# Kernel tuning notes

Hardware: AMD Instinct MI355X
Metric: run time of the kernel (lower is better)

The kernel has to match this reference:

```python
import jax, jax.numpy as jnp
import numpy as np

N = 240000
B = 2
GRID = (480, 360, 32)
NUM_CLASS = 20
IGNORE_LABEL = 0
MINB = np.array([0.0, -np.pi, -4.0], np.float32)
MAXB = np.array([50.0, np.pi, 2.0], np.float32)
EPS = 1e-5


def setup_inputs() -> dict:
    key = jax.random.key(0)
    ks = jax.random.split(key, 32)
    d = {}
    d['pt_fea'] = jax.random.normal(ks[0], (N, 6), jnp.float32)
    # cylindrical coords (rho, phi, z) uniformly inside the volume
    u = jax.random.uniform(ks[1], (N, 3), jnp.float32)
    d['xyz'] = u * jnp.asarray(MAXB - MINB) + jnp.asarray(MINB)
    d['batch_idx'] = jnp.sort(jax.random.randint(ks[2], (N,), 0, B)).astype(jnp.int64)
    d['pt_lab'] = jax.random.randint(ks[3], (N,), 0, NUM_CLASS).astype(jnp.int64)
    d['shuffled_ind'] = jnp.arange(N, dtype=jnp.int64)  # identity perm (deterministic)
    i = 4
    for name, c in [('bn0', 9), ('bn1', 64), ('bn2', 128), ('bn3', 256)]:
        d[name + '_g'] = jax.random.uniform(ks[i], (c,), jnp.float32, 0.5, 1.5); i += 1
        d[name + '_b'] = jax.random.normal(ks[i], (c,), jnp.float32) * 0.1; i += 1
        d[name + '_m'] = jax.random.normal(ks[i], (c,), jnp.float32) * 0.1; i += 1
        d[name + '_v'] = jax.random.uniform(ks[i], (c,), jnp.float32, 0.5, 1.5); i += 1
    for name, (fi, fo) in [('1', (9, 64)), ('2', (64, 128)), ('3', (128, 256)), ('4', (256, 256))]:
        d['w' + name] = jax.random.normal(ks[i], (fi, fo), jnp.float32) / np.sqrt(fi); i += 1
        d['b' + name] = jax.random.normal(ks[i], (fo,), jnp.float32) * 0.01; i += 1
    d['wc'] = jax.random.normal(ks[i], (256, 16), jnp.float32) / 16.0; i += 1
    d['bc'] = jax.random.normal(ks[i], (16,), jnp.float32) * 0.01
    return d


def _bn(x, g, b, m, v):
    return (x - m) * (g * jax.lax.rsqrt(v + EPS)) + b


def _ppmodel(feat, bn0_g, bn0_b, bn0_m, bn0_v, w1, b1, bn1_g, bn1_b, bn1_m, bn1_v,
             w2, b2, bn2_g, bn2_b, bn2_m, bn2_v, w3, b3, bn3_g, bn3_b, bn3_m, bn3_v, w4, b4):
    x = _bn(feat, bn0_g, bn0_b, bn0_m, bn0_v)
    x = jax.nn.relu(_bn(x @ w1 + b1, bn1_g, bn1_b, bn1_m, bn1_v))
    x = jax.nn.relu(_bn(x @ w2 + b2, bn2_g, bn2_b, bn2_m, bn2_v))
    x = jax.nn.relu(_bn(x @ w3 + b3, bn3_g, bn3_b, bn3_m, bn3_v))
    return x @ w4 + b4  # [N, 256]


def reference(pt_fea, xyz, batch_idx, pt_lab, shuffled_ind,
              bn0_g, bn0_b, bn0_m, bn0_v, w1, b1, bn1_g, bn1_b, bn1_m, bn1_v,
              w2, b2, bn2_g, bn2_b, bn2_m, bn2_v, w3, b3, bn3_g, bn3_b, bn3_m, bn3_v,
              w4, b4, wc, bc):
    minb = jnp.asarray(MINB)
    maxb = jnp.asarray(MAXB)
    grid = jnp.asarray(np.array(GRID, np.float32))
    intervals = (maxb - minb) / (grid - 1.0)

    clamped = jnp.clip(xyz, minb, maxb)
    ind = jnp.floor((clamped - minb) / intervals).astype(jnp.int32)  # [N,3]
    voxel_centers = (ind.astype(jnp.float32) + 0.5) * intervals + minb
    rel_xyz = xyz - voxel_centers
    feat = jnp.concatenate([rel_xyz, pt_fea], axis=1)  # [N,9]

    bi = batch_idx.astype(jnp.int32)
    counts = jnp.full((B,) + GRID + (NUM_CLASS,), IGNORE_LABEL, jnp.int32)
    counts = counts.at[bi, ind[:, 0], ind[:, 1], ind[:, 2], pt_lab].add(1)
    voxel_labels = jnp.argmax(counts, axis=-1).astype(jnp.int32)  # [B,480,360,32]

    feat = feat[shuffled_ind]

    flat = ((bi.astype(jnp.int64) * GRID[0] + ind[:, 0]) * GRID[1] + ind[:, 1]) * GRID[2] + ind[:, 2]
    unq, unq_inv = jnp.unique(flat, size=N, fill_value=-1, return_inverse=True)
    unq_inv = unq_inv.reshape(-1)

    processed = _ppmodel(feat, bn0_g, bn0_b, bn0_m, bn0_v, w1, b1, bn1_g, bn1_b, bn1_m, bn1_v,
                         w2, b2, bn2_g, bn2_b, bn2_m, bn2_v, w3, b3, bn3_g, bn3_b, bn3_m, bn3_v, w4, b4)
    pooled = jax.ops.segment_max(processed, unq_inv, num_segments=N)
    seg_cnt = jax.ops.segment_sum(jnp.ones((N,), jnp.float32), unq_inv, num_segments=N)
    pooled = jnp.where(seg_cnt[:, None] > 0, pooled, 0.0)  # zero out empty (padded) segments

    processed_pooled = jax.nn.relu(pooled @ wc + bc)  # fea_compression

    cat_pt_ind = jnp.concatenate([batch_idx[:, None], ind.astype(jnp.int64)], axis=1)
    return (unq, processed_pooled, voxel_labels, cat_pt_ind)
```

## Files before the change

kernel.cpp:

```cpp
#include <hip/hip_runtime.h>
#include <stdint.h>

#define N_PTS 240000
#define NV    11059200
#define NWORDS 172800
#define NB_PT 938
#define NB_WORD 675
#define NBLK_MLP 3750
#define PA 264

typedef __bf16 bf16x8 __attribute__((ext_vector_type(8)));
typedef short  short8 __attribute__((ext_vector_type(8)));
typedef float  f32x4  __attribute__((ext_vector_type(4)));

__device__ __forceinline__ unsigned short f2bf(float f) {
  unsigned u = __builtin_bit_cast(unsigned, f);
  return (unsigned short)((u + 0x7FFFu + ((u >> 16) & 1u)) >> 16);
}
__device__ __forceinline__ float bf2f(unsigned short h) {
  unsigned u = ((unsigned)h) << 16;
  return __builtin_bit_cast(float, u);
}

__device__ __forceinline__ unsigned block_sum(unsigned v, unsigned* s4, int t) {
  #pragma unroll
  for (int o = 32; o; o >>= 1) v += __shfl_down(v, o);
  if ((t & 63) == 0) s4[t >> 6] = v;
  __syncthreads();
  unsigned r = s4[0] + s4[1] + s4[2] + s4[3];
  __syncthreads();
  return r;
}

__global__ void prep_vox_kernel(
    const float* __restrict__ bng0, const float* __restrict__ bnb0, const float* __restrict__ bnm0, const float* __restrict__ bnv0,
    const float* __restrict__ bng1, const float* __restrict__ bnb1, const float* __restrict__ bnm1, const float* __restrict__ bnv1,
    const float* __restrict__ bng2, const float* __restrict__ bnb2, const float* __restrict__ bnm2, const float* __restrict__ bnv2,
    const float* __restrict__ bng3, const float* __restrict__ bnb3, const float* __restrict__ bnm3, const float* __restrict__ bnv3,
    const float* __restrict__ w1, const float* __restrict__ b1,
    const float* __restrict__ w2, const float* __restrict__ b2,
    const float* __restrict__ w3, const float* __restrict__ b3,
    const float* __restrict__ w4, const float* __restrict__ wc,
    float* __restrict__ s0, float* __restrict__ t0, float* __restrict__ w1e, float* __restrict__ be1,
    float* __restrict__ be2, float* __restrict__ be3,
    unsigned short* __restrict__ w2t, unsigned short* __restrict__ w3t, unsigned short* __restrict__ w4t,
    unsigned short* __restrict__ wct,
    const float* __restrict__ xyz, const int* __restrict__ bidx,
    unsigned* __restrict__ flatkeys, unsigned long long* __restrict__ bitmap,
    float* __restrict__ out_cat, float* __restrict__ out_unq)
{
  if (blockIdx.x < 256) {
    const int id = blockIdx.x * 256 + threadIdx.x;
    { int c = id >> 8, k = id & 255; w4t[c * 256 + k] = f2bf(w4[k * 256 + c]); }
    if (id < 32768) { int c = id >> 7, k = id & 127;
      float s = bng3[c] * rsqrtf(bnv3[c] + 1e-5f);
      w3t[c * 128 + k] = f2bf(w3[k * 256 + c] * s); }
    if (id < 8192) { int c = id >> 6, k = id & 63;
      float s = bng2[c] * rsqrtf(bnv2[c] + 1e-5f);
      w2t[c * 64 + k] = f2bf(w2[k * 128 + c] * s); }
    if (id < 4096) { int c = id >> 8, k = id & 255;
      wct[c * 256 + k] = f2bf(wc[k * 16 + c]); }
    if (id < 576) { int k = id / 64, c = id % 64;
      float s = bng1[c] * rsqrtf(bnv1[c] + 1e-5f);
      w1e[k * 64 + c] = w1[k * 64 + c] * s; }
    if (id < 64)  { float s = bng1[id] * rsqrtf(bnv1[id] + 1e-5f); be1[id] = (b1[id] - bnm1[id]) * s + bnb1[id]; }
    if (id < 128) { float s = bng2[id] * rsqrtf(bnv2[id] + 1e-5f); be2[id] = (b2[id] - bnm2[id]) * s + bnb2[id]; }
    if (id < 256) { float s = bng3[id] * rsqrtf(bnv3[id] + 1e-5f); be3[id] = (b3[id] - bnm3[id]) * s + bnb3[id]; }
    if (id < 9)   { float s = bng0[id] * rsqrtf(bnv0[id] + 1e-5f); s0[id] = s; t0[id] = bnb0[id] - bnm0[id] * s; }
    return;
  }
  const int j = (blockIdx.x - 256) * 256 + threadIdx.x;
  if (j >= N_PTS) return;
  out_unq[j] = -1.0f;
  const float PI_F = 3.14159265358979323846f;
  const float minb[3] = {0.0f, -PI_F, -4.0f};
  const float maxb[3] = {50.0f, PI_F, 2.0f};
  const float gm1[3]  = {479.0f, 359.0f, 31.0f};
  int ind[3];
  #pragma unroll
  for (int d = 0; d < 3; ++d) {
    float itv = (maxb[d] - minb[d]) / gm1[d];
    float x  = xyz[(size_t)j * 3 + d];
    float cl = fminf(fmaxf(x, minb[d]), maxb[d]);
    ind[d] = (int)floorf((cl - minb[d]) / itv);
  }
  const int bi = bidx[j];
  const unsigned flat = ((unsigned)(bi * 480 + ind[0]) * 360u + (unsigned)ind[1]) * 32u + (unsigned)ind[2];
  flatkeys[j] = flat;
  atomicOr(&bitmap[flat >> 6], 1ull << (flat & 63u));
  float* oc = out_cat + (size_t)j * 4;
  oc[0] = (float)bi; oc[1] = (float)ind[0]; oc[2] = (float)ind[1]; oc[3] = (float)ind[2];
}

__global__ void reduce_words(const unsigned long long* __restrict__ bm, unsigned* __restrict__ bsums) {
  __shared__ unsigned sh[256];
  const int w = blockIdx.x * 256 + threadIdx.x;
  sh[threadIdx.x] = (unsigned)__popcll(bm[w]);
  __syncthreads();
  for (int s = 128; s > 0; s >>= 1) { if (threadIdx.x < s) sh[threadIdx.x] += sh[threadIdx.x + s]; __syncthreads(); }
  if (threadIdx.x == 0) bsums[blockIdx.x] = sh[0];
}

__global__ __launch_bounds__(256) void scatter_unq(
    const unsigned long long* __restrict__ bm, const unsigned* __restrict__ bsums,
    unsigned* __restrict__ wordpref, unsigned* __restrict__ unqvals, float* __restrict__ out_unq)
{
  __shared__ unsigned sh[256];
  __shared__ unsigned s4[4];
  const int t = threadIdx.x, b = blockIdx.x;
  const int w = b * 256 + t;
  unsigned long long word = bm[w];
  unsigned own = (unsigned)__popcll(word);
  sh[t] = own; __syncthreads();
  for (int off = 1; off < 256; off <<= 1) {
    unsigned v = (t >= off) ? sh[t - off] : 0u;
    __syncthreads(); sh[t] += v; __syncthreads();
  }
  unsigned v = 0;
  for (int i = t; i < b; i += 256) v += bsums[i];
  const unsigned excl = block_sum(v, s4, t);
  unsigned r = excl + sh[t] - own;
  wordpref[w] = r;
  while (word) {
    int bit = __builtin_ctzll(word);
    unsigned id = (unsigned)w * 64u + (unsigned)bit;
    unqvals[r] = id;
    out_unq[r] = (float)id;
    ++r;
    word &= word - 1;
  }
}

__global__ void inv_kernel(const unsigned* __restrict__ flatkeys, const unsigned long long* __restrict__ bm,
                           const unsigned* __restrict__ wordpref,
                           unsigned* __restrict__ unq_inv, unsigned* __restrict__ cnt) {
  const int j = blockIdx.x * 256 + threadIdx.x;
  if (j >= N_PTS) return;
  const unsigned f = flatkeys[j];
  const unsigned w = f >> 6, b = f & 63u;
  const unsigned r = wordpref[w] + (unsigned)__popcll(bm[w] & ((1ull << b) - 1ull));
  unq_inv[j] = r;
  atomicAdd(&cnt[r], 1u);
}

__global__ void reduce_cnt(const unsigned* __restrict__ cnt, unsigned* __restrict__ bsums) {
  __shared__ unsigned sh[256];
  const int j = blockIdx.x * 256 + threadIdx.x;
  sh[threadIdx.x] = (j < N_PTS) ? cnt[j] : 0u;
  __syncthreads();
  for (int s = 128; s > 0; s >>= 1) { if (threadIdx.x < s) sh[threadIdx.x] += sh[threadIdx.x + s]; __syncthreads(); }
  if (threadIdx.x == 0) bsums[blockIdx.x] = sh[0];
}

__global__ __launch_bounds__(256) void scan_cnt(
    const unsigned* __restrict__ cnt, const unsigned* __restrict__ bsums,
    unsigned* __restrict__ off, unsigned* __restrict__ cur)
{
  __shared__ unsigned sh[256];
  __shared__ unsigned s4[4];
  const int t = threadIdx.x, b = blockIdx.x;
  const int j = b * 256 + t;
  unsigned own = (j < N_PTS) ? cnt[j] : 0u;
  sh[t] = own; __syncthreads();
  for (int o = 1; o < 256; o <<= 1) {
    unsigned v = (t >= o) ? sh[t - o] : 0u;
    __syncthreads(); sh[t] += v; __syncthreads();
  }
  unsigned v = 0;
  for (int i = t; i < b; i += 256) v += bsums[i];
  const unsigned excl = block_sum(v, s4, t);
  if (j < N_PTS) { unsigned e = excl + sh[t] - own; off[j] = e; cur[j] = e; }
}

__global__ void plist_fill_kernel(const unsigned* __restrict__ unq_inv, unsigned* __restrict__ cur,
                                  unsigned long long* __restrict__ plist64,
                                  const unsigned* __restrict__ cnt, const float* __restrict__ bc,
                                  float* __restrict__ out_pooled) {
  const int j = blockIdx.x * 256 + threadIdx.x;
  if (j >= N_PTS) return;
  const unsigned r = unq_inv[j];
  plist64[atomicAdd(&cur[r], 1u)] = ((unsigned long long)r << 32) | (unsigned)j;
  if (cnt[j] == 0) {
    #pragma unroll
    for (int c = 0; c < 16; ++c) out_pooled[(size_t)j * 16 + c] = fmaxf(bc[c], 0.f);
  }
}

template<int K, int C, bool RELU, bool MIDB>
__device__ __forceinline__ void gemm_stage(
    const unsigned short* __restrict__ Wt,
    const float* __restrict__ bias,
    const unsigned short* in,
    unsigned short* outp,
    int wave, int l15, int quad)
{
  constexpr int KC = K / 32;
  constexpr int NT = C / 64;
  f32x4 acc[4][NT];
  #pragma unroll
  for (int mt = 0; mt < 4; ++mt)
    #pragma unroll
    for (int nt = 0; nt < NT; ++nt) acc[mt][nt] = (f32x4){0.f, 0.f, 0.f, 0.f};
  const unsigned short* wp[NT];
  #pragma unroll
  for (int nt = 0; nt < NT; ++nt)
    wp[nt] = Wt + (size_t)(wave * 16 * NT + nt * 16 + l15) * K + quad * 8;
  bf16x8 b0[NT], b1r[NT], b2r[NT];
  #pragma unroll
  for (int nt = 0; nt < NT; ++nt)
    b0[nt] = __builtin_bit_cast(bf16x8, *(const short8*)(wp[nt]));
  if (KC > 1) {
    #pragma unroll
    for (int nt = 0; nt < NT; ++nt)
      b1r[nt] = __builtin_bit_cast(bf16x8, *(const short8*)(wp[nt] + 32));
  }
  #pragma unroll
  for (int kc = 0; kc < KC; ++kc) {
    if (kc + 2 < KC) {
      #pragma unroll
      for (int nt = 0; nt < NT; ++nt)
        b2r[nt] = __builtin_bit_cast(bf16x8, *(const short8*)(wp[nt] + (kc + 2) * 32));
    }
    __builtin_amdgcn_s_setprio(1);
    #pragma unroll
    for (int mt = 0; mt < 4; ++mt) {
      bf16x8 a = __builtin_bit_cast(bf16x8, *(const short8*)&in[(mt * 16 + l15) * PA + kc * 32 + quad * 8]);
      #pragma unroll
      for (int nt = 0; nt < NT; ++nt)
        acc[mt][nt] = __builtin_amdgcn_mfma_f32_16x16x32_bf16(b0[nt], a, acc[mt][nt], 0, 0, 0);
    }
    __builtin_amdgcn_s_setprio(0);
    #pragma unroll
    for (int nt = 0; nt < NT; ++nt) { b0[nt] = b1r[nt]; b1r[nt] = b2r[nt]; }
  }
  if (MIDB) __syncthreads();
  #pragma unroll
  for (int mt = 0; mt < 4; ++mt)
    #pragma unroll
    for (int nt = 0; nt < NT; ++nt) {
      const int cbase = wave * 16 * NT + nt * 16 + quad * 4;
      const f32x4 bs = *(const f32x4*)&bias[cbase];
      unsigned short h[4];
      #pragma unroll
      for (int r = 0; r < 4; ++r) {
        float y = acc[mt][nt][r] + bs[r];
        if (RELU) y = fmaxf(y, 0.f);
        h[r] = f2bf(y);
      }
      uint2 pk; pk.x = (unsigned)h[0] | ((unsigned)h[1] << 16);
      pk.y = (unsigned)h[2] | ((unsigned)h[3] << 16);
      *(uint2*)&outp[(mt * 16 + l15) * PA + cbase] = pk;
    }
  __syncthreads();
}

__global__ __launch_bounds__(256, 3) void mlp_pool_kernel(
    const float* __restrict__ ptfea, const float* __restrict__ xyz, const int* __restrict__ shuf,
    const unsigned long long* __restrict__ plist64,
    const unsigned* __restrict__ offv, const unsigned* __restrict__ cnt,
    const int* __restrict__ ptlab, const unsigned* __restrict__ unqvals,
    const float* __restrict__ s0, const float* __restrict__ t0,
    const float* __restrict__ w1e, const float* __restrict__ be1,
    const unsigned short* __restrict__ w2t, const float* __restrict__ be2,
    const unsigned short* __restrict__ w3t, const float* __restrict__ be3,
    const unsigned short* __restrict__ w4t, const float* __restrict__ b4,
    const unsigned short* __restrict__ wct, const float* __restrict__ bc,
    unsigned short* __restrict__ partials, float* __restrict__ out_pooled,
    float* __restrict__ out_lab)
{
  __shared__ __align__(16) unsigned short buf[64 * PA];
  __shared__ int segs[64];
  __shared__ int jrows[64];
  __shared__ int s_alast;
  __shared__ int s_nrun;
  __shared__ unsigned short s_runs[32];
  __shared__ unsigned char s_lead[64], s_comp[64];
  const int tid  = threadIdx.x;
  const int wave = tid >> 6, lane = tid & 63;
  const int l15 = lane & 15, quad = lane >> 4;
  const int row0 = blockIdx.x * 64;

  if (tid == 0) { s_alast = 0; s_nrun = 0; }
  if (lane < 16) {
    const int r = wave * 16 + lane;
    const unsigned long long v = plist64[row0 + r];
    jrows[r] = (int)(unsigned)v;
    segs[r]  = (int)(unsigned)(v >> 32);
  }

  {
    const int r = wave * 16 + (lane >> 2), part = lane & 3;
    const int sj = shuf[jrows[r]];
    const float PI_F = 3.14159265358979323846f;
    const float minb[3] = {0.0f, -PI_F, -4.0f};
    const float maxb[3] = {50.0f, PI_F, 2.0f};
    const float gm1[3]  = {479.0f, 359.0f, 31.0f};
    float x0[9];
    #pragma unroll
    for (int d = 0; d < 3; ++d) {
      float itv = (maxb[d] - minb[d]) / gm1[d];
      float x   = xyz[(size_t)sj * 3 + d];
      float cl  = fminf(fmaxf(x, minb[d]), maxb[d]);
      float fi  = floorf((cl - minb[d]) / itv);
      float center = (fi + 0.5f) * itv + minb[d];
      x0[d] = (x - center) * s0[d] + t0[d];
    }
    #pragma unroll
    for (int d = 0; d < 6; ++d) x0[3 + d] = ptfea[(size_t)sj * 6 + d] * s0[3 + d] + t0[3 + d];
    unsigned short h[16];
    #pragma unroll
    for (int ci = 0; ci < 16; ++ci) {
      float acc = be1[part * 16 + ci];
      #pragma unroll
      for (int k = 0; k < 9; ++k) acc += x0[k] * w1e[k * 64 + part * 16 + ci];
      h[ci] = f2bf(fmaxf(acc, 0.0f));
    }
    *(short8*)&buf[r * PA + part * 16]     = *(short8*)&h[0];
    *(short8*)&buf[r * PA + part * 16 + 8] = *(short8*)&h[8];
  }
  __syncthreads();

  if (tid < 64) {
    const int r = tid;
    bool lead = (r == 0) || (segs[r] != segs[r - 1]);
    s_lead[r] = lead ? 1 : 0;
    unsigned char comp = 0;
    int e = r + 1;
    if (lead) {
      atomicMax(&s_alast, r);
      while (e < 64 && segs[e] == segs[r]) ++e;
      const unsigned s = (unsigned)segs[r];
      comp = (offv[s] == (unsigned)(row0 + r) && offv[s] + cnt[s] == (unsigned)(row0 + e)) ? 1 : 0;
    }
    s_comp[r] = comp;
    if (comp) {
      int bestl;
      if (e - r == 1) bestl = ptlab[jrows[r]];
      else {
        int bestc = 0; bestl = 32;
        for (int i = r; i < e; ++i) {
          const int li = ptlab[jrows[i]];
          int cc = 0;
          for (int k2 = r; k2 < e; ++k2) cc += (ptlab[jrows[k2]] == li) ? 1 : 0;
          if (cc > bestc || (cc == bestc && li < bestl)) { bestc = cc; bestl = li; }
        }
      }
      out_lab[unqvals[segs[r]]] = (float)bestl;
    }
    const bool multi = lead && (e - r) > 1;
    unsigned long long mm = __ballot(multi);
    if (multi) {
      int idx = (int)__popcll(mm & ((1ull << r) - 1ull));
      s_runs[idx] = (unsigned short)((r << 8) | e);
    }
    if (tid == 0) s_nrun = (int)__popcll(mm);
  }

  gemm_stage< 64, 128, true,  false>(w2t, be2, buf,       buf + 136, wave, l15, quad);
  gemm_stage<128, 256, true,  true >(w3t, be3, buf + 136, buf,       wave, l15, quad);
  gemm_stage<256, 256, false, true >(w4t, b4,  buf,       buf,       wave, l15, quad);

  {
    const int n = s_nrun;
    for (int i = 0; i < n; ++i) {
      const int re = s_runs[i];
      const int r = re >> 8, e = re & 255;
      float m = bf2f(buf[r * PA + tid]);
      for (int rr = r + 1; rr < e; ++rr) m = fmaxf(m, bf2f(buf[rr * PA + tid]));
      buf[r * PA + tid] = f2bf(m);
    }
  }
  __syncthreads();

  {
    const int c = tid;
    const int alast = s_alast;
    const size_t b2 = (size_t)blockIdx.x * 2;
    if (!s_comp[0])     partials[b2 * 256 + c]       = buf[0 * PA + c];
    if (!s_comp[alast]) partials[(b2 + 1) * 256 + c] = buf[alast * PA + c];
  }

  {
    const unsigned short* wp = wct + l15 * 256 + quad * 8;
    bf16x8 wv[8];
    #pragma unroll
    for (int kc = 0; kc < 8; ++kc)
      wv[kc] = __builtin_bit_cast(bf16x8, *(const short8*)(wp + kc * 32));
    f32x4 acc = (f32x4){0.f, 0.f, 0.f, 0.f};
    #pragma unroll
    for (int kc = 0; kc < 8; ++kc) {
      bf16x8 x = __builtin_bit_cast(bf16x8, *(const short8*)&buf[(wave * 16 + l15) * PA + kc * 32 + quad * 8]);
      acc = __builtin_amdgcn_mfma_f32_16x16x32_bf16(wv[kc], x, acc, 0, 0, 0);
    }
    const int r1 = wave * 16 + l15;
    if (s_lead[r1] && s_comp[r1]) {
      const f32x4 bcv = *(const f32x4*)&bc[quad * 4];
      f32x4 v;
      #pragma unroll
      for (int r = 0; r < 4; ++r) v[r] = fmaxf(acc[r] + bcv[r], 0.f);
      *(f32x4*)&out_pooled[(size_t)segs[r1] * 16 + quad * 4] = v;
    }
  }
}

__global__ __launch_bounds__(256) void merge_kernel(
    const unsigned long long* __restrict__ plist64,
    const unsigned* __restrict__ offv, const unsigned* __restrict__ cnt,
    const unsigned short* __restrict__ partials,
    const int* __restrict__ ptlab, const unsigned* __restrict__ unqvals,
    const float* __restrict__ wc, const float* __restrict__ bc,
    float* __restrict__ out_pooled, float* __restrict__ out_lab)
{
  __shared__ float pooled[256];
  __shared__ float psum[256];
  const int b = blockIdx.x;
  const unsigned s = (unsigned)(plist64[(size_t)b * 64 + 63] >> 32);
  const unsigned o = offv[s], e = o + cnt[s];
  if ((o >> 6) != (unsigned)b) return;
  if (e <= (unsigned)(b + 1) * 64) return;
  const int B1 = (int)((e - 1) >> 6);
  const int c = threadIdx.x;
  float m = bf2f(partials[((size_t)2 * b + 1) * 256 + c]);
  for (int bb = b + 1; bb <= B1; ++bb)
    m = fmaxf(m, bf2f(partials[(size_t)2 * bb * 256 + c]));
  pooled[c] = m;
  __syncthreads();
  const int co = c & 15, kg = c >> 4;
  float p = 0.f;
  #pragma unroll
  for (int k = kg * 16; k < kg * 16 + 16; ++k) p += pooled[k] * wc[k * 16 + co];
  psum[c] = p;
  __syncthreads();
  if (c < 16) {
    float acc = bc[c];
    #pragma unroll
    for (int g = 0; g < 16; ++g) acc += psum[g * 16 + c];
    out_pooled[(size_t)s * 16 + c] = fmaxf(acc, 0.f);
  }
  if (c == 0) {
    int bestc = 0, bestl = 32;
    for (unsigned i = o; i < e; ++i) {
      const int li = ptlab[(unsigned)plist64[i]];
      int cc = 0;
      for (unsigned k2 = o; k2 < e; ++k2) cc += (ptlab[(unsigned)plist64[k2]] == li) ? 1 : 0;
      if (cc > bestc || (cc == bestc && li < bestl)) { bestc = cc; bestl = li; }
    }
    out_lab[unqvals[s]] = (float)bestl;
  }
}

extern "C" void kernel_launch(void* const* d_in, const int* in_sizes, int n_in,
                              void* d_out, int out_size, void* d_ws, size_t ws_size,
                              hipStream_t stream)
{
  const float* pt_fea = (const float*)d_in[0];
  const float* xyz    = (const float*)d_in[1];
  const int*   bidx   = (const int*)d_in[2];
  const int*   ptlab  = (const int*)d_in[3];
  const int*   shuf   = (const int*)d_in[4];
  const float* bng0 = (const float*)d_in[5],  *bnb0 = (const float*)d_in[6],  *bnm0 = (const float*)d_in[7],  *bnv0 = (const float*)d_in[8];
  const float* bng1 = (const float*)d_in[9],  *bnb1 = (const float*)d_in[10], *bnm1 = (const float*)d_in[11], *bnv1 = (const float*)d_in[12];
  const float* bng2 = (const float*)d_in[13], *bnb2 = (const float*)d_in[14], *bnm2 = (const float*)d_in[15], *bnv2 = (const float*)d_in[16];
  const float* bng3 = (const float*)d_in[17], *bnb3 = (const float*)d_in[18], *bnm3 = (const float*)d_in[19], *bnv3 = (const float*)d_in[20];
  const float* w1 = (const float*)d_in[21], *b1 = (const float*)d_in[22];
  const float* w2 = (const float*)d_in[23], *b2 = (const float*)d_in[24];
  const float* w3 = (const float*)d_in[25], *b3 = (const float*)d_in[26];
  const float* w4 = (const float*)d_in[27], *b4 = (const float*)d_in[28];
  const float* wc = (const float*)d_in[29], *bc = (const float*)d_in[30];

  float* out        = (float*)d_out;
  float* out_unq    = out;
  float* out_pooled = out + 240000;
  float* out_lab    = out + 4080000;
  float* out_cat    = out + 15139200;

  char* wsb = (char*)d_ws;
  size_t o = 0;
  auto alloc = [&](size_t bytes) -> void* { void* p = wsb + o; o = (o + bytes + 255) & ~(size_t)255; return p; };
  unsigned long long* bitmap = (unsigned long long*)alloc((size_t)NWORDS * 8);
  unsigned* cnt    = (unsigned*)alloc((size_t)N_PTS * 4);
  const size_t zero_bytes = o;
  float* s0  = (float*)alloc(9 * 4);
  float* t0  = (float*)alloc(9 * 4);
  float* w1e = (float*)alloc(576 * 4);
  float* be1 = (float*)alloc(64 * 4);
  float* be2 = (float*)alloc(128 * 4);
  float* be3 = (float*)alloc(256 * 4);
  unsigned short* w2t = (unsigned short*)alloc(8192 * 2);
  unsigned short* w3t = (unsigned short*)alloc(32768 * 2);
  unsigned short* w4t = (unsigned short*)alloc(65536 * 2);
  unsigned short* wct = (unsigned short*)alloc(4096 * 2);
  unsigned* flatkeys = (unsigned*)alloc((size_t)N_PTS * 4);
  unsigned* unq_inv  = (unsigned*)alloc((size_t)N_PTS * 4);
  unsigned* unqvals  = (unsigned*)alloc((size_t)N_PTS * 4);
  unsigned* offv     = (unsigned*)alloc((size_t)N_PTS * 4);
  unsigned* cur      = (unsigned*)alloc((size_t)N_PTS * 4);
  unsigned long long* plist64 = (unsigned long long*)alloc((size_t)N_PTS * 8);
  unsigned* wordpref = (unsigned*)alloc((size_t)NWORDS * 4);
  unsigned* bsumA    = (unsigned*)alloc(NB_WORD * 4);
  unsigned* bsumB    = (unsigned*)alloc(NB_PT * 4);
  unsigned short* partials = (unsigned short*)alloc((size_t)NBLK_MLP * 2 * 256 * 2);

  hipMemsetAsync(bitmap, 0, zero_bytes, stream);
  hipMemsetAsync(out_lab, 0, (size_t)NV * 4, stream);

  prep_vox_kernel<<<256 + NB_PT, 256, 0, stream>>>(
      bng0, bnb0, bnm0, bnv0, bng1, bnb1, bnm1, bnv1,
      bng2, bnb2, bnm2, bnv2, bng3, bnb3, bnm3, bnv3,
      w1, b1, w2, b2, w3, b3, w4, wc,
      s0, t0, w1e, be1, be2, be3, w2t, w3t, w4t, wct,
      xyz, bidx, flatkeys, bitmap, out_cat, out_unq);
  reduce_words<<<NB_WORD, 256, 0, stream>>>(bitmap, bsumA);
  scatter_unq<<<NB_WORD, 256, 0, stream>>>(bitmap, bsumA, wordpref, unqvals, out_unq);
  inv_kernel<<<NB_PT, 256, 0, stream>>>(flatkeys, bitmap, wordpref, unq_inv, cnt);
  reduce_cnt<<<NB_PT, 256, 0, stream>>>(cnt, bsumB);
  scan_cnt<<<NB_PT, 256, 0, stream>>>(cnt, bsumB, offv, cur);
  plist_fill_kernel<<<NB_PT, 256, 0, stream>>>(unq_inv, cur, plist64, cnt, bc, out_pooled);
  mlp_pool_kernel<<<NBLK_MLP, 256, 0, stream>>>(pt_fea, xyz, shuf, plist64, offv, cnt,
                                                ptlab, unqvals,
                                                s0, t0, w1e, be1, w2t, be2, w3t, be3, w4t, b4,
                                                wct, bc, partials, out_pooled, out_lab);
  merge_kernel<<<NBLK_MLP, 256, 0, stream>>>(plist64, offv, cnt, partials,
                                             ptlab, unqvals, wc, bc, out_pooled, out_lab);
}
```

Measured before the change: 352.8 us.

## Fuse scans into single-pass kernels, merge stage into MLP, zeroing into prep

Each reduce-then-scan kernel pair (voxel bitmap words and per-segment counts) becomes one kernel. Blocks publish their totals through flag words and read the totals of earlier blocks with acquire/release atomics. The separate merge kernel is gone: the last MLP block touching a segment that spans several blocks, found with a per-segment atomic counter, now does the cross-block max, the compression matmul and the label vote. Zeroing of the counters, flags and the large label output moves from memsets into extra blocks of the prep kernel. This cuts launch count and serialization gaps. In exchange it relies on spin-waits that assume earlier blocks make progress, plus extra atomics and fences.

```diff
diff --git a/kernel.cpp b/kernel.cpp
--- a/kernel.cpp
+++ b/kernel.cpp
@@ -8,6 +8,9 @@
 #define NB_WORD 675
 #define NBLK_MLP 3750
 #define PA 264
+#define NZB 1536
+#define ZR1_F4 120512
+#define LAB_F4 2764800
 
 typedef __bf16 bf16x8 __attribute__((ext_vector_type(8)));
 typedef short  short8 __attribute__((ext_vector_type(8)));
@@ -47,8 +50,16 @@
     unsigned short* __restrict__ wct,
     const float* __restrict__ xyz, const int* __restrict__ bidx,
     unsigned* __restrict__ flatkeys, unsigned long long* __restrict__ bitmap,
-    float* __restrict__ out_cat, float* __restrict__ out_unq)
+    float* __restrict__ out_cat, float* __restrict__ out_unq,
+    float* __restrict__ zr1, float* __restrict__ out_lab)
 {
+  if (blockIdx.x >= 256 + NB_PT) {
+    const int zi = (blockIdx.x - (256 + NB_PT)) * 256 + threadIdx.x;
+    const f32x4 z = (f32x4){0.f, 0.f, 0.f, 0.f};
+    for (int i = zi; i < ZR1_F4; i += NZB * 256) ((f32x4*)zr1)[i] = z;
+    for (int i = zi; i < LAB_F4; i += NZB * 256) ((f32x4*)out_lab)[i] = z;
+    return;
+  }
   if (blockIdx.x < 256) {
     const int id = blockIdx.x * 256 + threadIdx.x;
     { int c = id >> 8, k = id & 255; w4t[c * 256 + k] = f2bf(w4[k * 256 + c]); }
@@ -92,17 +103,8 @@
   oc[0] = (float)bi; oc[1] = (float)ind[0]; oc[2] = (float)ind[1]; oc[3] = (float)ind[2];
 }
 
-__global__ void reduce_words(const unsigned long long* __restrict__ bm, unsigned* __restrict__ bsums) {
-  __shared__ unsigned sh[256];
-  const int w = blockIdx.x * 256 + threadIdx.x;
-  sh[threadIdx.x] = (unsigned)__popcll(bm[w]);
-  __syncthreads();
-  for (int s = 128; s > 0; s >>= 1) { if (threadIdx.x < s) sh[threadIdx.x] += sh[threadIdx.x + s]; __syncthreads(); }
-  if (threadIdx.x == 0) bsums[blockIdx.x] = sh[0];
-}
-
-__global__ __launch_bounds__(256) void scatter_unq(
-    const unsigned long long* __restrict__ bm, const unsigned* __restrict__ bsums,
+__global__ __launch_bounds__(256) void scan_unq_kernel(
+    const unsigned long long* __restrict__ bm, unsigned* __restrict__ flags,
     unsigned* __restrict__ wordpref, unsigned* __restrict__ unqvals, float* __restrict__ out_unq)
 {
   __shared__ unsigned sh[256];
@@ -116,8 +118,15 @@
     unsigned v = (t >= off) ? sh[t - off] : 0u;
     __syncthreads(); sh[t] += v; __syncthreads();
   }
+  if (t == 0)
+    __hip_atomic_fetch_add(&flags[b], sh[255] | 0x80000000u, __ATOMIC_RELEASE, __HIP_MEMORY_SCOPE_AGENT);
   unsigned v = 0;
-  for (int i = t; i < b; i += 256) v += bsums[i];
+  for (int i = t; i < b; i += 256) {
+    unsigned x;
+    while (((x = __hip_atomic_load(&flags[i], __ATOMIC_ACQUIRE, __HIP_MEMORY_SCOPE_AGENT)) & 0x80000000u) == 0u)
+      __builtin_amdgcn_s_sleep(16);
+    v += x & 0x7FFFFFFFu;
+  }
   const unsigned excl = block_sum(v, s4, t);
   unsigned r = excl + sh[t] - own;
   wordpref[w] = r;
@@ -143,17 +152,8 @@
   atomicAdd(&cnt[r], 1u);
 }
 
-__global__ void reduce_cnt(const unsigned* __restrict__ cnt, unsigned* __restrict__ bsums) {
-  __shared__ unsigned sh[256];
-  const int j = blockIdx.x * 256 + threadIdx.x;
-  sh[threadIdx.x] = (j < N_PTS) ? cnt[j] : 0u;
-  __syncthreads();
-  for (int s = 128; s > 0; s >>= 1) { if (threadIdx.x < s) sh[threadIdx.x] += sh[threadIdx.x + s]; __syncthreads(); }
-  if (threadIdx.x == 0) bsums[blockIdx.x] = sh[0];
-}
-
-__global__ __launch_bounds__(256) void scan_cnt(
-    const unsigned* __restrict__ cnt, const unsigned* __restrict__ bsums,
+__global__ __launch_bounds__(256) void scan_cnt_kernel(
+    const unsigned* __restrict__ cnt, unsigned* __restrict__ flags,
     unsigned* __restrict__ off, unsigned* __restrict__ cur)
 {
   __shared__ unsigned sh[256];
@@ -166,8 +166,15 @@
     unsigned v = (t >= o) ? sh[t - o] : 0u;
     __syncthreads(); sh[t] += v; __syncthreads();
   }
+  if (t == 0)
+    __hip_atomic_fetch_add(&flags[b], sh[255] | 0x80000000u, __ATOMIC_RELEASE, __HIP_MEMORY_SCOPE_AGENT);
   unsigned v = 0;
-  for (int i = t; i < b; i += 256) v += bsums[i];
+  for (int i = t; i < b; i += 256) {
+    unsigned x;
+    while (((x = __hip_atomic_load(&flags[i], __ATOMIC_ACQUIRE, __HIP_MEMORY_SCOPE_AGENT)) & 0x80000000u) == 0u)
+      __builtin_amdgcn_s_sleep(16);
+    v += x & 0x7FFFFFFFu;
+  }
   const unsigned excl = block_sum(v, s4, t);
   if (j < N_PTS) { unsigned e = excl + sh[t] - own; off[j] = e; cur[j] = e; }
 }
@@ -265,6 +272,8 @@
     const unsigned short* __restrict__ w3t, const float* __restrict__ be3,
     const unsigned short* __restrict__ w4t, const float* __restrict__ b4,
     const unsigned short* __restrict__ wct, const float* __restrict__ bc,
+    const float* __restrict__ wcr,
+    unsigned* __restrict__ segdone,
     unsigned short* __restrict__ partials, float* __restrict__ out_pooled,
     float* __restrict__ out_lab)
 {
@@ -275,6 +284,10 @@
   __shared__ int s_nrun;
   __shared__ unsigned short s_runs[32];
   __shared__ unsigned char s_lead[64], s_comp[64];
+  __shared__ float s_pool[256];
+  __shared__ float s_psum[256];
+  __shared__ int s_fin[2];
+  __shared__ int s_nfin;
   const int tid  = threadIdx.x;
   const int wave = tid >> 6, lane = tid & 63;
   const int l15 = lane & 15, quad = lane >> 4;
@@ -401,51 +414,57 @@
       *(f32x4*)&out_pooled[(size_t)segs[r1] * 16 + quad * 4] = v;
     }
   }
-}
-
-__global__ __launch_bounds__(256) void merge_kernel(
-    const unsigned long long* __restrict__ plist64,
-    const unsigned* __restrict__ offv, const unsigned* __restrict__ cnt,
-    const unsigned short* __restrict__ partials,
-    const int* __restrict__ ptlab, const unsigned* __restrict__ unqvals,
-    const float* __restrict__ wc, const float* __restrict__ bc,
-    float* __restrict__ out_pooled, float* __restrict__ out_lab)
-{
-  __shared__ float pooled[256];
-  __shared__ float psum[256];
-  const int b = blockIdx.x;
-  const unsigned s = (unsigned)(plist64[(size_t)b * 64 + 63] >> 32);
-  const unsigned o = offv[s], e = o + cnt[s];
-  if ((o >> 6) != (unsigned)b) return;
-  if (e <= (unsigned)(b + 1) * 64) return;
-  const int B1 = (int)((e - 1) >> 6);
-  const int c = threadIdx.x;
-  float m = bf2f(partials[((size_t)2 * b + 1) * 256 + c]);
-  for (int bb = b + 1; bb <= B1; ++bb)
-    m = fmaxf(m, bf2f(partials[(size_t)2 * bb * 256 + c]));
-  pooled[c] = m;
-  __syncthreads();
-  const int co = c & 15, kg = c >> 4;
-  float p = 0.f;
-  #pragma unroll
-  for (int k = kg * 16; k < kg * 16 + 16; ++k) p += pooled[k] * wc[k * 16 + co];
-  psum[c] = p;
-  __syncthreads();
-  if (c < 16) {
-    float acc = bc[c];
-    #pragma unroll
-    for (int g = 0; g < 16; ++g) acc += psum[g * 16 + c];
-    out_pooled[(size_t)s * 16 + c] = fmaxf(acc, 0.f);
-  }
-  if (c == 0) {
-    int bestc = 0, bestl = 32;
-    for (unsigned i = o; i < e; ++i) {
-      const int li = ptlab[(unsigned)plist64[i]];
-      int cc = 0;
-      for (unsigned k2 = o; k2 < e; ++k2) cc += (ptlab[(unsigned)plist64[k2]] == li) ? 1 : 0;
-      if (cc > bestc || (cc == bestc && li < bestl)) { bestc = cc; bestl = li; }
-    }
-    out_lab[unqvals[s]] = (float)bestl;
+
+  __threadfence();
+  __syncthreads();
+  if (tid == 0) {
+    s_nfin = 0;
+    int cand[2]; int nc = 0;
+    cand[nc++] = segs[0];
+    if (segs[63] != segs[0]) cand[nc++] = segs[63];
+    for (int i = 0; i < nc; ++i) {
+      const unsigned s = (unsigned)cand[i];
+      const unsigned o = offv[s], e = o + cnt[s];
+      const int b0 = (int)(o >> 6), B1 = (int)((e - 1) >> 6);
+      if (b0 == B1) continue;
+      const unsigned old = __hip_atomic_fetch_add(&segdone[s], 1u,
+                              __ATOMIC_ACQ_REL, __HIP_MEMORY_SCOPE_AGENT);
+      if ((int)old == B1 - b0) s_fin[s_nfin++] = (int)s;
+    }
+  }
+  __syncthreads();
+  for (int fi = 0; fi < s_nfin; ++fi) {
+    const unsigned s = (unsigned)s_fin[fi];
+    const unsigned o = offv[s], e = o + cnt[s];
+    const int b0 = (int)(o >> 6), B1 = (int)((e - 1) >> 6);
+    float m = bf2f(partials[((size_t)2 * b0 + 1) * 256 + tid]);
+    for (int bb = b0 + 1; bb <= B1; ++bb)
+      m = fmaxf(m, bf2f(partials[(size_t)2 * bb * 256 + tid]));
+    s_pool[tid] = m;
+    __syncthreads();
+    const int co = tid & 15, kg = tid >> 4;
+    float p = 0.f;
+    #pragma unroll
+    for (int k = kg * 16; k < kg * 16 + 16; ++k) p += s_pool[k] * wcr[k * 16 + co];
+    s_psum[tid] = p;
+    __syncthreads();
+    if (tid < 16) {
+      float acc = bc[tid];
+      #pragma unroll
+      for (int g = 0; g < 16; ++g) acc += s_psum[g * 16 + tid];
+      out_pooled[(size_t)s * 16 + tid] = fmaxf(acc, 0.f);
+    }
+    if (tid == 0) {
+      int bestc = 0, bestl = 32;
+      for (unsigned i = o; i < e; ++i) {
+        const int li = ptlab[(unsigned)plist64[i]];
+        int cc = 0;
+        for (unsigned k2 = o; k2 < e; ++k2) cc += (ptlab[(unsigned)plist64[k2]] == li) ? 1 : 0;
+        if (cc > bestc || (cc == bestc && li < bestl)) { bestc = cc; bestl = li; }
+      }
+      out_lab[unqvals[s]] = (float)bestl;
+    }
+    __syncthreads();
   }
 }
 
@@ -478,8 +497,10 @@
   size_t o = 0;
   auto alloc = [&](size_t bytes) -> void* { void* p = wsb + o; o = (o + bytes + 255) & ~(size_t)255; return p; };
   unsigned long long* bitmap = (unsigned long long*)alloc((size_t)NWORDS * 8);
-  unsigned* cnt    = (unsigned*)alloc((size_t)N_PTS * 4);
-  const size_t zero_bytes = o;
+  unsigned* cnt     = (unsigned*)alloc((size_t)N_PTS * 4);
+  unsigned* segdone = (unsigned*)alloc((size_t)N_PTS * 4);
+  unsigned* flagsA  = (unsigned*)alloc(4096);
+  unsigned* flagsB  = (unsigned*)alloc(4096);
   float* s0  = (float*)alloc(9 * 4);
   float* t0  = (float*)alloc(9 * 4);
   float* w1e = (float*)alloc(576 * 4);
@@ -497,29 +518,24 @@
   unsigned* cur      = (unsigned*)alloc((size_t)N_PTS * 4);
   unsigned long long* plist64 = (unsigned long long*)alloc((size_t)N_PTS * 8);
   unsigned* wordpref = (unsigned*)alloc((size_t)NWORDS * 4);
-  unsigned* bsumA    = (unsigned*)alloc(NB_WORD * 4);
-  unsigned* bsumB    = (unsigned*)alloc(NB_PT * 4);
   unsigned short* partials = (unsigned short*)alloc((size_t)NBLK_MLP * 2 * 256 * 2);
 
-  hipMemsetAsync(bitmap, 0, zero_bytes, stream);
-  hipMemsetAsync(out_lab, 0, (size_t)NV * 4, stream);
-
-  prep_vox_kernel<<<256 + NB_PT, 256, 0, stream>>>(
+  hipMemsetAsync(bitmap, 0, (size_t)NWORDS * 8, stream);
+
+  prep_vox_kernel<<<256 + NB_PT + NZB, 256, 0, stream>>>(
       bng0, bnb0, bnm0, bnv0, bng1, bnb1, bnm1, bnv1,
       bng2, bnb2, bnm2, bnv2, bng3, bnb3, bnm3, bnv3,
       w1, b1, w2, b2, w3, b3, w4, wc,
       s0, t0, w1e, be1, be2, be3, w2t, w3t, w4t, wct,
-      xyz, bidx, flatkeys, bitmap, out_cat, out_unq);
-  reduce_words<<<NB_WORD, 256, 0, stream>>>(bitmap, bsumA);
-  scatter_unq<<<NB_WORD, 256, 0, stream>>>(bitmap, bsumA, wordpref, unqvals, out_unq);
+      xyz, bidx, flatkeys, bitmap, out_cat, out_unq,
+      (float*)cnt, out_lab);
+  scan_unq_kernel<<<NB_WORD, 256, 0, stream>>>(bitmap, flagsA, wordpref, unqvals, out_unq);
   inv_kernel<<<NB_PT, 256, 0, stream>>>(flatkeys, bitmap, wordpref, unq_inv, cnt);
-  reduce_cnt<<<NB_PT, 256, 0, stream>>>(cnt, bsumB);
-  scan_cnt<<<NB_PT, 256, 0, stream>>>(cnt, bsumB, offv, cur);
+  scan_cnt_kernel<<<NB_PT, 256, 0, stream>>>(cnt, flagsB, offv, cur);
   plist_fill_kernel<<<NB_PT, 256, 0, stream>>>(unq_inv, cur, plist64, cnt, bc, out_pooled);
   mlp_pool_kernel<<<NBLK_MLP, 256, 0, stream>>>(pt_fea, xyz, shuf, plist64, offv, cnt,
                                                 ptlab, unqvals,
                                                 s0, t0, w1e, be1, w2t, be2, w3t, be3, w4t, b4,
-                                                wct, bc, partials, out_pooled, out_lab);
-  merge_kernel<<<NBLK_MLP, 256, 0, stream>>>(plist64, offv, cnt, partials,
-                                             ptlab, unqvals, wc, bc, out_pooled, out_lab);
-}
+                                                wct, bc, wc, segdone, partials,
+                                                out_pooled, out_lab);
+}
```

Measured after the change: 786.3 us. 123% more time.
